# Kernel tuning notes

Hardware: AMD Instinct MI355X
Metric: run time of the kernel (lower is better)

## Reference

```python
import jax, jax.numpy as jnp
import numpy as np

VOCAB = 50000
D = 256        # embedding_dim = nb_head * size_per_head
H = 8          # nb_head
DH = 32        # size_per_head
B = 8192
L = 64


def setup_inputs() -> dict:
    key = jax.random.key(0)
    ks = jax.random.split(key, 8)
    tokens = jax.random.randint(ks[0], (B, L), 0, VOCAB)
    scale = 0.02
    emb_table = jax.random.normal(ks[1], (VOCAB, D), dtype=jnp.float32) * scale
    WQ = jax.random.normal(ks[2], (D, D), dtype=jnp.float32) * scale
    WK = jax.random.normal(ks[3], (D, D), dtype=jnp.float32) * scale
    WV = jax.random.normal(ks[4], (D, D), dtype=jnp.float32) * scale
    WO = jax.random.normal(ks[5], (D, D), dtype=jnp.float32) * scale
    dense_w = jax.random.normal(ks[6], (D, 1), dtype=jnp.float32) * scale
    dense_b = jnp.zeros((1,), dtype=jnp.float32)
    return {"tokens": tokens, "emb_table": emb_table, "WQ": WQ, "WK": WK,
            "WV": WV, "WO": WO, "dense_w": dense_w, "dense_b": dense_b}


def _fastformer(x, WQ, WK, WV, WO):
    # x: [B, L, D]
    b, l, _ = x.shape
    Q = (x @ WQ).reshape(b, l, H, DH)
    K = (x @ WK).reshape(b, l, H, DH)
    V = (x @ WV).reshape(b, l, H, DH)
    global_q = jnp.mean(Q, axis=1, keepdims=True)   # [B,1,H,DH]
    global_k = jnp.mean(K, axis=1, keepdims=True)
    w = jnp.sum(global_q * K + global_k * Q, axis=-1)  # [B,L,H]
    w = jax.nn.softmax(w, axis=1)                       # softmax over seq
    context = (w[..., None] * V).reshape(b, l, D)
    return context @ WO


def reference(tokens, emb_table, WQ, WK, WV, WO, dense_w, dense_b):
    # NewsEncoder forward (inference: dropout = identity; masks computed but
    # unused by Fastformer.call, matching the original code).
    title_emb = emb_table[tokens]                       # [B,L,D]
    hidden = _fastformer(title_emb, WQ, WK, WV, WO)     # [B,L,D]
    scores = (hidden @ dense_w + dense_b)[..., 0]       # [B,L]
    attn = jax.nn.softmax(scores, axis=1)               # over seq
    news_vector = jnp.sum(hidden * attn[..., None], axis=1)  # [B,D]
    return news_vector
```

## Files before the change

### kernel.cpp

```cpp
#include <hip/hip_runtime.h>
#include <cstdint>


using f32x4  = __attribute__((ext_vector_type(4))) float;
using bf16x8 = __attribute__((ext_vector_type(8))) short;

__device__ __forceinline__ unsigned int pack2bf(float a, float b) {
  unsigned int ua = __builtin_bit_cast(unsigned int, a);
  unsigned int ub = __builtin_bit_cast(unsigned int, b);
  ua = (ua + 0x7fffu + ((ua >> 16) & 1u)) >> 16;
  ub = (ub + 0x7fffu + ((ub >> 16) & 1u)) >> 16;
  return ua | (ub << 16);
}
__device__ __forceinline__ unsigned short bf1(float a) {
  unsigned int ua = __builtin_bit_cast(unsigned int, a);
  ua = (ua + 0x7fffu + ((ua >> 16) & 1u)) >> 16;
  return (unsigned short)ua;
}
__device__ __forceinline__ float ubf(unsigned int u) {
  return __builtin_bit_cast(float, u << 16);
}
__device__ __forceinline__ void gload_lds16(const void* g, void* l) {
  __builtin_amdgcn_global_load_lds(
      (const __attribute__((address_space(1))) void*)g,
      (__attribute__((address_space(3))) void*)l, 16, 0, 0);
}

__global__ __launch_bounds__(256) void prep_kernel(const float* __restrict__ WV,
                                                   const float* __restrict__ WO,
                                                   const float* __restrict__ dw,
                                                   unsigned short* __restrict__ mbf) {
  __shared__ float wod[256];
  const int t = threadIdx.x;
  float acc = 0.f;
  for (int e = 0; e < 256; e += 4) {
    const float4 w4 = *(const float4*)(WO + (size_t)t * 256 + e);
    const float4 d4 = *(const float4*)(dw + e);
    acc += w4.x * d4.x + w4.y * d4.y + w4.z * d4.z + w4.w * d4.w;
  }
  wod[t] = acc;
  __syncthreads();
  for (int h = 0; h < 8; ++h) {
    float a = 0.f;
    for (int j = 0; j < 32; j += 4) {
      const float4 w4 = *(const float4*)(WV + (size_t)t * 256 + h * 32 + j);
      a += w4.x * wod[h*32+j] + w4.y * wod[h*32+j+1] + w4.z * wod[h*32+j+2] + w4.w * wod[h*32+j+3];
    }
    const float o = __shfl_xor(a, 1);
    if (!(t & 1)) ((unsigned int*)mbf)[h * 128 + (t >> 1)] = pack2bf(a, o);
  }
}

__global__ __launch_bounds__(256) void prep_T(const float* __restrict__ WQ,
                                              const float* __restrict__ WK,
                                              unsigned short* __restrict__ tkn) {
  __shared__ float ek[8][32], eq[8][32];
  const int t = threadIdx.x;
  const int n0 = blockIdx.x * 8;
  const int h  = n0 >> 8;
  {
    const int ei = t >> 5, j = t & 31;
    const int e = (n0 & 255) + ei;
    ek[ei][j] = WK[(size_t)e * 256 + h * 32 + j];
    eq[ei][j] = WQ[(size_t)e * 256 + h * 32 + j];
  }
  __syncthreads();
  float wqd[32], wkd[32];
#pragma unroll
  for (int j = 0; j < 32; j += 4) {
    *(float4*)(wqd + j) = *(const float4*)(WQ + (size_t)t * 256 + h * 32 + j);
    *(float4*)(wkd + j) = *(const float4*)(WK + (size_t)t * 256 + h * 32 + j);
  }
#pragma unroll
  for (int ei = 0; ei < 8; ++ei) {
    float a = 0.f;
#pragma unroll
    for (int j = 0; j < 32; ++j) a += wqd[j] * ek[ei][j] + wkd[j] * eq[ei][j];
    const float o = __shfl_xor(a, 1);
    if (!(t & 1)) ((unsigned int*)tkn)[(size_t)(n0 + ei) * 128 + (t >> 1)] = pack2bf(a, o);
  }
}

__global__ __launch_bounds__(256) void prep_P(const float* __restrict__ WV,
                                              const float* __restrict__ WO,
                                              unsigned short* __restrict__ ptb) {
  __shared__ float wvs[32][32];
  __shared__ float wos[32][256];
  const int t = threadIdx.x;
  const int h = blockIdx.x, d0 = blockIdx.y * 32;
  {
    const int dd = t >> 3, jq = (t & 7) * 4;
    *(float4*)(&wvs[dd][jq]) = *(const float4*)(WV + (size_t)(d0 + dd) * 256 + h * 32 + jq);
    const int c4 = (t & 63) * 4;
#pragma unroll
    for (int jj = 0; jj < 8; ++jj) {
      const int j = (t >> 6) * 8 + jj;
      *(float4*)(&wos[j][c4]) = *(const float4*)(WO + (size_t)(h * 32 + j) * 256 + c4);
    }
  }
  __syncthreads();
  const int n = t;
#pragma unroll 4
  for (int dd = 0; dd < 32; ++dd) {
    float a = 0.f;
#pragma unroll
    for (int j = 0; j < 32; ++j) a += wvs[dd][j] * wos[j][n];
    ptb[(size_t)n * 2048 + h * 256 + d0 + dd] = bf1(a);
  }
}

__global__ __launch_bounds__(256) void ebf_kernel(const float4* __restrict__ emb4,
                                                  uint2* __restrict__ out2, int n) {
  for (int i = blockIdx.x * 256 + threadIdx.x; i < n; i += gridDim.x * 256) {
    const float4 v = emb4[i];
    uint2 pk;
    pk.x = pack2bf(v.x, v.y);
    pk.y = pack2bf(v.z, v.w);
    out2[i] = pk;
  }
}

__global__ __launch_bounds__(256) void xbar_kernel(const int* __restrict__ tokens,
                                                   const unsigned short* __restrict__ ebf,
                                                   unsigned short* __restrict__ xbf) {
  __shared__ int tok[64];
  __shared__ float part[4][64][4];
  const int b = blockIdx.x, t = threadIdx.x;
  if (t < 64) tok[t] = tokens[b * 64 + t];
  __syncthreads();
  const int cp = t & 63, rg = t >> 6;
  const uint2* e2 = (const uint2*)ebf;
  float s0 = 0.f, s1 = 0.f, s2 = 0.f, s3 = 0.f;
#pragma unroll
  for (int ri = 0; ri < 16; ++ri) {
    const uint2 u = e2[(size_t)tok[rg * 16 + ri] * 64 + cp];
    s0 += ubf(u.x & 0xffffu); s1 += ubf(u.x >> 16);
    s2 += ubf(u.y & 0xffffu); s3 += ubf(u.y >> 16);
  }
  *(float4*)part[rg][cp] = make_float4(s0, s1, s2, s3);
  __syncthreads();
  if (t < 64) {
    const float4 p0 = *(const float4*)part[0][t];
    const float4 p1 = *(const float4*)part[1][t];
    const float4 p2 = *(const float4*)part[2][t];
    const float4 p3 = *(const float4*)part[3][t];
    const float a0 = (p0.x + p1.x + p2.x + p3.x) * (1.f / 64.f);
    const float a1 = (p0.y + p1.y + p2.y + p3.y) * (1.f / 64.f);
    const float a2 = (p0.z + p1.z + p2.z + p3.z) * (1.f / 64.f);
    const float a3 = (p0.w + p1.w + p2.w + p3.w) * (1.f / 64.f);
    uint2 pk;
    pk.x = pack2bf(a0, a1);
    pk.y = pack2bf(a2, a3);
    *(uint2*)((unsigned int*)xbf + (size_t)b * 128 + 2 * t) = pk;
  }
}

__global__ __launch_bounds__(256) void cgemm(const unsigned short* __restrict__ xbf,
                                             const unsigned short* __restrict__ tkn,
                                             unsigned short* __restrict__ cbf) {
  __shared__ unsigned short As[64 * 264];
  const int t = threadIdx.x;
  const int m0 = blockIdx.x * 64, n0 = blockIdx.y * 64;
#pragma unroll
  for (int it = 0; it < 8; ++it) {
    const int idx = it * 256 + t;
    const int row = idx >> 5, c = idx & 31;
    const uint4 v = *(const uint4*)(xbf + (size_t)(m0 + row) * 256 + c * 8);
    *(uint4*)(As + row * 264 + c * 8) = v;
  }
  __syncthreads();
  const int wv = t >> 6, l = t & 63;
  const int g = l >> 4, r = l & 15;
#pragma unroll
  for (int nt = 0; nt < 4; ++nt) {
    const int n = n0 + nt * 16 + r;
    f32x4 acc = {0.f, 0.f, 0.f, 0.f};
#pragma unroll
    for (int kk = 0; kk < 8; ++kk) {
      const bf16x8 a  = *(const bf16x8*)(As + (16 * wv + r) * 264 + kk * 32 + g * 8);
      const bf16x8 bb = *(const bf16x8*)(tkn + (size_t)n * 256 + kk * 32 + g * 8);
      acc = __builtin_amdgcn_mfma_f32_16x16x32_bf16(a, bb, acc, 0, 0, 0);
    }
#pragma unroll
    for (int i = 0; i < 4; ++i)
      cbf[(size_t)(m0 + 16 * wv + g * 4 + i) * 2048 + n] = bf1(acc[i]);
  }
}

__global__ __launch_bounds__(256) void main_kernel(const int* __restrict__ tokens,
                                                   const unsigned short* __restrict__ ebf,
                                                   const unsigned short* __restrict__ mbf,
                                                   const float* __restrict__ dense_b,
                                                   unsigned short* __restrict__ cbf) {
  __shared__ unsigned short xl[64 * 256];
  __shared__ float wslds[64 * 17];
  __shared__ unsigned short cfT[16 * 80];
  const int t = threadIdx.x;
  const int b = blockIdx.x;
  const int wv = t >> 6, l = t & 63;
  const int g = l >> 4, r = l & 15;
  {
    unsigned int* cz = (unsigned int*)(cfT + 8 * 80);
    for (int z = t; z < 320; z += 256) cz[z] = 0u;
  }
  {
    const int ln = t & 63;
#pragma unroll
    for (int it = 0; it < 8; ++it) {
      const int R0 = it * 8 + wv * 2;
      const int R  = R0 + (ln >> 5);
      const int j  = ln & 31;
      const int tk = tokens[b * 64 + R];
      const unsigned short* src = ebf + (size_t)tk * 256 + ((j ^ (R & 7)) << 3);
      gload_lds16(src, (void*)(xl + R0 * 256));
    }
  }
  __syncthreads();
  {
    const unsigned short* arow = xl + (16 * wv + r) * 256;
    const int sw = r & 7;
    const unsigned short* brow = (r < 8) ? (cbf + (size_t)b * 2048 + r * 256)
                                         : (mbf + (size_t)(r - 8) * 256);
    f32x4 acc = {0.f, 0.f, 0.f, 0.f};
#pragma unroll
    for (int kk = 0; kk < 8; ++kk) {
      const bf16x8 a  = *(const bf16x8*)(arow + (((kk * 4 + g) ^ sw) << 3));
      const bf16x8 bb = *(const bf16x8*)(brow + kk * 32 + g * 8);
      acc = __builtin_amdgcn_mfma_f32_16x16x32_bf16(a, bb, acc, 0, 0, 0);
    }
#pragma unroll
    for (int i = 0; i < 4; ++i)
      wslds[(16 * wv + g * 4 + i) * 17 + r] = acc[i];
  }
  __syncthreads();
  {
#pragma unroll
    for (int hh = 0; hh < 2; ++hh) {
      const int h = 2 * wv + hh;
      const float v = wslds[l * 17 + h];
      float mx = v;
#pragma unroll
      for (int sft = 32; sft; sft >>= 1) mx = fmaxf(mx, __shfl_xor(mx, sft));
      const float e = expf(v - mx);
      float sm = e;
#pragma unroll
      for (int sft = 32; sft; sft >>= 1) sm += __shfl_xor(sm, sft);
      wslds[l * 17 + h] = e / sm;
    }
  }
  __syncthreads();
  {
    float p[8], sv[8];
#pragma unroll
    for (int h = 0; h < 8; ++h) { p[h] = wslds[l*17 + h]; sv[h] = wslds[l*17 + 8 + h]; }
    float sc = dense_b[0];
#pragma unroll
    for (int h = 0; h < 8; ++h) sc += p[h] * sv[h];
    float mx = sc;
#pragma unroll
    for (int sft = 32; sft; sft >>= 1) mx = fmaxf(mx, __shfl_xor(mx, sft));
    const float e = expf(sc - mx);
    float sm = e;
#pragma unroll
    for (int sft = 32; sft; sft >>= 1) sm += __shfl_xor(sm, sft);
    const float attn = e / sm;
    float cc0, cc1;
    if      (wv == 0) { cc0 = attn * p[0]; cc1 = attn * p[1]; }
    else if (wv == 1) { cc0 = attn * p[2]; cc1 = attn * p[3]; }
    else if (wv == 2) { cc0 = attn * p[4]; cc1 = attn * p[5]; }
    else              { cc0 = attn * p[6]; cc1 = attn * p[7]; }
    cfT[(2 * wv) * 80 + l]     = bf1(cc0);
    cfT[(2 * wv + 1) * 80 + l] = bf1(cc1);
  }
  __syncthreads();
  {
    const bf16x8 a0 = *(const bf16x8*)(cfT + r * 80 + g * 8);
    const bf16x8 a1 = *(const bf16x8*)(cfT + r * 80 + 32 + g * 8);
    const short* xs = (const short*)xl;
#pragma unroll
    for (int nt = 0; nt < 4; ++nt) {
      const int d = wv * 64 + nt * 16 + r;
      short bv0[8], bv1[8];
#pragma unroll
      for (int j = 0; j < 8; ++j) {
        const int off = ((((d >> 3) ^ j) << 3) | (d & 7));
        bv0[j] = xs[(g * 8 + j) * 256 + off];
        bv1[j] = xs[(32 + g * 8 + j) * 256 + off];
      }
      f32x4 acc = {0.f, 0.f, 0.f, 0.f};
      acc = __builtin_amdgcn_mfma_f32_16x16x32_bf16(a0, *(const bf16x8*)bv0, acc, 0, 0, 0);
      acc = __builtin_amdgcn_mfma_f32_16x16x32_bf16(a1, *(const bf16x8*)bv1, acc, 0, 0, 0);
      if (g < 2) {
#pragma unroll
        for (int i = 0; i < 4; ++i) {
          const int h = g * 4 + i;
          cbf[(size_t)b * 2048 + h * 256 + d] = bf1(acc[i]);
        }
      }
    }
  }
}

__global__ __launch_bounds__(256) void pgemm(const unsigned short* __restrict__ cbf,
                                             const unsigned short* __restrict__ ptb,
                                             float* __restrict__ out) {
  __shared__ unsigned short As[32 * 264];
  const int t = threadIdx.x;
  const int m0 = blockIdx.x * 32, n0 = blockIdx.y * 64;
  const int wv = t >> 6, l = t & 63;
  const int g = l >> 4, r = l & 15;
  const int msub = wv & 1, nhalf = wv >> 1;
  f32x4 acc[2] = {};
  for (int kc = 0; kc < 8; ++kc) {
    __syncthreads();
#pragma unroll
    for (int it = 0; it < 4; ++it) {
      const int idx = it * 256 + t;
      const int row = idx >> 5, c = idx & 31;
      const uint4 v = *(const uint4*)(cbf + (size_t)(m0 + row) * 2048 + kc * 256 + c * 8);
      *(uint4*)(As + row * 264 + c * 8) = v;
    }
    __syncthreads();
#pragma unroll
    for (int kk = 0; kk < 8; ++kk) {
      const bf16x8 a = *(const bf16x8*)(As + (16 * msub + r) * 264 + kk * 32 + g * 8);
#pragma unroll
      for (int nt = 0; nt < 2; ++nt) {
        const int n = n0 + (nhalf * 2 + nt) * 16 + r;
        const bf16x8 bb = *(const bf16x8*)(ptb + (size_t)n * 2048 + kc * 256 + kk * 32 + g * 8);
        acc[nt] = __builtin_amdgcn_mfma_f32_16x16x32_bf16(a, bb, acc[nt], 0, 0, 0);
      }
    }
  }
#pragma unroll
  for (int nt = 0; nt < 2; ++nt) {
    const int n = n0 + (nhalf * 2 + nt) * 16 + r;
#pragma unroll
    for (int i = 0; i < 4; ++i)
      out[(size_t)(m0 + 16 * msub + g * 4 + i) * 256 + n] = acc[nt][i];
  }
}

extern "C" void kernel_launch(void* const* d_in, const int* in_sizes, int n_in,
                              void* d_out, int out_size, void* d_ws, size_t ws_size,
                              hipStream_t stream) {
  const int*   tokens = (const int*)d_in[0];
  const float* emb    = (const float*)d_in[1];
  const float* WQ     = (const float*)d_in[2];
  const float* WK     = (const float*)d_in[3];
  const float* WV     = (const float*)d_in[4];
  const float* WO     = (const float*)d_in[5];
  const float* dw     = (const float*)d_in[6];
  const float* db     = (const float*)d_in[7];
  float* out = (float*)d_out;

  unsigned short* base = (unsigned short*)d_ws;
  unsigned short* mbf  = base;
  unsigned short* xbf  = base + 2048;
  unsigned short* tkn  = xbf + (size_t)8192 * 256;
  unsigned short* cbf  = tkn + (size_t)2048 * 256;
  unsigned short* ebf  = cbf + (size_t)8192 * 2048;
  unsigned short* ptb  = ebf + (size_t)50000 * 256;

  const size_t need_bytes = (size_t)(2048 + 8192*256 + 2048*256 + 8192*2048
                                     + 50000*256 + 256*2048) * 2;
  if (ws_size < need_bytes) return;

  prep_kernel<<<dim3(1), dim3(256), 0, stream>>>(WV, WO, dw, mbf);
  prep_T<<<dim3(256), dim3(256), 0, stream>>>(WQ, WK, tkn);
  prep_P<<<dim3(8, 8), dim3(256), 0, stream>>>(WV, WO, ptb);
  ebf_kernel<<<dim3(2048), dim3(256), 0, stream>>>((const float4*)emb, (uint2*)ebf,
                                                   50000 * 64);
  xbar_kernel<<<dim3(8192), dim3(256), 0, stream>>>(tokens, ebf, xbf);
  cgemm<<<dim3(128, 32), dim3(256), 0, stream>>>(xbf, tkn, cbf);
  main_kernel<<<dim3(8192), dim3(256), 0, stream>>>(tokens, ebf, mbf, db, cbf);
  pgemm<<<dim3(256, 4), dim3(256), 0, stream>>>(cbf, ptb, out);
}
```

Measured before the change: 275.1 us.

## Merge weight-prep kernels, widen xbar gathers, rotate store order in main kernel

The three small weight-preprocessing kernels are merged into one launch that dispatches on block index, removing two kernel launches and letting their blocks run concurrently. The xbar mean-gather kernel now loads 16-byte rows over 8 row groups instead of 8-byte rows over 4, and reduces through a larger shared buffer. In the main kernel the per-lane tile order is rotated by lane index so the scattered bf16 stores and LDS reads spread across addresses. The merged kernel reserves the largest shared-memory footprint for every block, and the wider gather uses more LDS.

```diff
diff --git a/kernel.cpp b/kernel.cpp
--- a/kernel.cpp
+++ b/kernel.cpp
@@ -26,86 +26,84 @@
       (__attribute__((address_space(3))) void*)l, 16, 0, 0);
 }
 
-__global__ __launch_bounds__(256) void prep_kernel(const float* __restrict__ WV,
-                                                   const float* __restrict__ WO,
-                                                   const float* __restrict__ dw,
-                                                   unsigned short* __restrict__ mbf) {
-  __shared__ float wod[256];
+__global__ __launch_bounds__(256) void prep_all(const float* __restrict__ WQ,
+                                                const float* __restrict__ WK,
+                                                const float* __restrict__ WV,
+                                                const float* __restrict__ WO,
+                                                const float* __restrict__ dw,
+                                                unsigned short* __restrict__ mbf,
+                                                unsigned short* __restrict__ tkn,
+                                                unsigned short* __restrict__ ptb) {
   const int t = threadIdx.x;
-  float acc = 0.f;
-  for (int e = 0; e < 256; e += 4) {
-    const float4 w4 = *(const float4*)(WO + (size_t)t * 256 + e);
-    const float4 d4 = *(const float4*)(dw + e);
-    acc += w4.x * d4.x + w4.y * d4.y + w4.z * d4.z + w4.w * d4.w;
-  }
-  wod[t] = acc;
-  __syncthreads();
-  for (int h = 0; h < 8; ++h) {
-    float a = 0.f;
+  const int bid = blockIdx.x;
+  if (bid == 0) {
+    __shared__ float wod[256];
+    float acc = 0.f;
+    for (int e = 0; e < 256; e += 4) {
+      const float4 w4 = *(const float4*)(WO + (size_t)t * 256 + e);
+      const float4 d4 = *(const float4*)(dw + e);
+      acc += w4.x * d4.x + w4.y * d4.y + w4.z * d4.z + w4.w * d4.w;
+    }
+    wod[t] = acc;
+    __syncthreads();
+    for (int h = 0; h < 8; ++h) {
+      float a = 0.f;
+      for (int j = 0; j < 32; j += 4) {
+        const float4 w4 = *(const float4*)(WV + (size_t)t * 256 + h * 32 + j);
+        a += w4.x * wod[h*32+j] + w4.y * wod[h*32+j+1] + w4.z * wod[h*32+j+2] + w4.w * wod[h*32+j+3];
+      }
+      const float o = __shfl_xor(a, 1);
+      if (!(t & 1)) ((unsigned int*)mbf)[h * 128 + (t >> 1)] = pack2bf(a, o);
+    }
+  } else if (bid <= 256) {
+    __shared__ float ek[8][32], eq[8][32];
+    const int n0 = (bid - 1) * 8;
+    const int h  = n0 >> 8;
+    {
+      const int ei = t >> 5, j = t & 31;
+      const int e = (n0 & 255) + ei;
+      ek[ei][j] = WK[(size_t)e * 256 + h * 32 + j];
+      eq[ei][j] = WQ[(size_t)e * 256 + h * 32 + j];
+    }
+    __syncthreads();
+    float wqd[32], wkd[32];
+#pragma unroll
     for (int j = 0; j < 32; j += 4) {
-      const float4 w4 = *(const float4*)(WV + (size_t)t * 256 + h * 32 + j);
-      a += w4.x * wod[h*32+j] + w4.y * wod[h*32+j+1] + w4.z * wod[h*32+j+2] + w4.w * wod[h*32+j+3];
-    }
-    const float o = __shfl_xor(a, 1);
-    if (!(t & 1)) ((unsigned int*)mbf)[h * 128 + (t >> 1)] = pack2bf(a, o);
-  }
-}
-
-__global__ __launch_bounds__(256) void prep_T(const float* __restrict__ WQ,
-                                              const float* __restrict__ WK,
-                                              unsigned short* __restrict__ tkn) {
-  __shared__ float ek[8][32], eq[8][32];
-  const int t = threadIdx.x;
-  const int n0 = blockIdx.x * 8;
-  const int h  = n0 >> 8;
-  {
-    const int ei = t >> 5, j = t & 31;
-    const int e = (n0 & 255) + ei;
-    ek[ei][j] = WK[(size_t)e * 256 + h * 32 + j];
-    eq[ei][j] = WQ[(size_t)e * 256 + h * 32 + j];
-  }
-  __syncthreads();
-  float wqd[32], wkd[32];
-#pragma unroll
-  for (int j = 0; j < 32; j += 4) {
-    *(float4*)(wqd + j) = *(const float4*)(WQ + (size_t)t * 256 + h * 32 + j);
-    *(float4*)(wkd + j) = *(const float4*)(WK + (size_t)t * 256 + h * 32 + j);
-  }
-#pragma unroll
-  for (int ei = 0; ei < 8; ++ei) {
-    float a = 0.f;
-#pragma unroll
-    for (int j = 0; j < 32; ++j) a += wqd[j] * ek[ei][j] + wkd[j] * eq[ei][j];
-    const float o = __shfl_xor(a, 1);
-    if (!(t & 1)) ((unsigned int*)tkn)[(size_t)(n0 + ei) * 128 + (t >> 1)] = pack2bf(a, o);
-  }
-}
-
-__global__ __launch_bounds__(256) void prep_P(const float* __restrict__ WV,
-                                              const float* __restrict__ WO,
-                                              unsigned short* __restrict__ ptb) {
-  __shared__ float wvs[32][32];
-  __shared__ float wos[32][256];
-  const int t = threadIdx.x;
-  const int h = blockIdx.x, d0 = blockIdx.y * 32;
-  {
-    const int dd = t >> 3, jq = (t & 7) * 4;
-    *(float4*)(&wvs[dd][jq]) = *(const float4*)(WV + (size_t)(d0 + dd) * 256 + h * 32 + jq);
-    const int c4 = (t & 63) * 4;
-#pragma unroll
-    for (int jj = 0; jj < 8; ++jj) {
-      const int j = (t >> 6) * 8 + jj;
-      *(float4*)(&wos[j][c4]) = *(const float4*)(WO + (size_t)(h * 32 + j) * 256 + c4);
-    }
-  }
-  __syncthreads();
-  const int n = t;
+      *(float4*)(wqd + j) = *(const float4*)(WQ + (size_t)t * 256 + h * 32 + j);
+      *(float4*)(wkd + j) = *(const float4*)(WK + (size_t)t * 256 + h * 32 + j);
+    }
+#pragma unroll
+    for (int ei = 0; ei < 8; ++ei) {
+      float a = 0.f;
+#pragma unroll
+      for (int j = 0; j < 32; ++j) a += wqd[j] * ek[ei][j] + wkd[j] * eq[ei][j];
+      const float o = __shfl_xor(a, 1);
+      if (!(t & 1)) ((unsigned int*)tkn)[(size_t)(n0 + ei) * 128 + (t >> 1)] = pack2bf(a, o);
+    }
+  } else {
+    __shared__ float wvs[32][32];
+    __shared__ float wos[32][256];
+    const int pb = bid - 257;
+    const int h = pb >> 3, d0 = (pb & 7) * 32;
+    {
+      const int dd = t >> 3, jq = (t & 7) * 4;
+      *(float4*)(&wvs[dd][jq]) = *(const float4*)(WV + (size_t)(d0 + dd) * 256 + h * 32 + jq);
+      const int c4 = (t & 63) * 4;
+#pragma unroll
+      for (int jj = 0; jj < 8; ++jj) {
+        const int j = (t >> 6) * 8 + jj;
+        *(float4*)(&wos[j][c4]) = *(const float4*)(WO + (size_t)(h * 32 + j) * 256 + c4);
+      }
+    }
+    __syncthreads();
+    const int n = t;
 #pragma unroll 4
-  for (int dd = 0; dd < 32; ++dd) {
-    float a = 0.f;
-#pragma unroll
-    for (int j = 0; j < 32; ++j) a += wvs[dd][j] * wos[j][n];
-    ptb[(size_t)n * 2048 + h * 256 + d0 + dd] = bf1(a);
+    for (int dd = 0; dd < 32; ++dd) {
+      float a = 0.f;
+#pragma unroll
+      for (int j = 0; j < 32; ++j) a += wvs[dd][j] * wos[j][n];
+      ptb[(size_t)n * 2048 + h * 256 + d0 + dd] = bf1(a);
+    }
   }
 }
 
@@ -124,35 +122,31 @@
                                                    const unsigned short* __restrict__ ebf,
                                                    unsigned short* __restrict__ xbf) {
   __shared__ int tok[64];
-  __shared__ float part[4][64][4];
+  __shared__ float part[8][256];
   const int b = blockIdx.x, t = threadIdx.x;
   if (t < 64) tok[t] = tokens[b * 64 + t];
   __syncthreads();
-  const int cp = t & 63, rg = t >> 6;
-  const uint2* e2 = (const uint2*)ebf;
-  float s0 = 0.f, s1 = 0.f, s2 = 0.f, s3 = 0.f;
-#pragma unroll
-  for (int ri = 0; ri < 16; ++ri) {
-    const uint2 u = e2[(size_t)tok[rg * 16 + ri] * 64 + cp];
-    s0 += ubf(u.x & 0xffffu); s1 += ubf(u.x >> 16);
-    s2 += ubf(u.y & 0xffffu); s3 += ubf(u.y >> 16);
-  }
-  *(float4*)part[rg][cp] = make_float4(s0, s1, s2, s3);
-  __syncthreads();
-  if (t < 64) {
-    const float4 p0 = *(const float4*)part[0][t];
-    const float4 p1 = *(const float4*)part[1][t];
-    const float4 p2 = *(const float4*)part[2][t];
-    const float4 p3 = *(const float4*)part[3][t];
-    const float a0 = (p0.x + p1.x + p2.x + p3.x) * (1.f / 64.f);
-    const float a1 = (p0.y + p1.y + p2.y + p3.y) * (1.f / 64.f);
-    const float a2 = (p0.z + p1.z + p2.z + p3.z) * (1.f / 64.f);
-    const float a3 = (p0.w + p1.w + p2.w + p3.w) * (1.f / 64.f);
-    uint2 pk;
-    pk.x = pack2bf(a0, a1);
-    pk.y = pack2bf(a2, a3);
-    *(uint2*)((unsigned int*)xbf + (size_t)b * 128 + 2 * t) = pk;
-  }
+  const int rg = t >> 5;
+  const int c16 = t & 31;
+  const uint4* e4 = (const uint4*)ebf;
+  float s[8] = {};
+#pragma unroll
+  for (int ri = 0; ri < 8; ++ri) {
+    const uint4 u = e4[(size_t)tok[rg * 8 + ri] * 32 + c16];
+    s[0] += ubf(u.x & 0xffffu); s[1] += ubf(u.x >> 16);
+    s[2] += ubf(u.y & 0xffffu); s[3] += ubf(u.y >> 16);
+    s[4] += ubf(u.z & 0xffffu); s[5] += ubf(u.z >> 16);
+    s[6] += ubf(u.w & 0xffffu); s[7] += ubf(u.w >> 16);
+  }
+#pragma unroll
+  for (int j = 0; j < 8; ++j) part[rg][c16 * 8 + j] = s[j];
+  __syncthreads();
+  float a = 0.f;
+#pragma unroll
+  for (int rg2 = 0; rg2 < 8; ++rg2) a += part[rg2][t];
+  a *= (1.f / 64.f);
+  const float o = __shfl_xor(a, 1);
+  if (!(t & 1)) ((unsigned int*)xbf)[(size_t)b * 128 + (t >> 1)] = pack2bf(a, o);
 }
 
 __global__ __launch_bounds__(256) void cgemm(const unsigned short* __restrict__ xbf,
@@ -278,7 +272,8 @@
     const bf16x8 a1 = *(const bf16x8*)(cfT + r * 80 + 32 + g * 8);
     const short* xs = (const short*)xl;
 #pragma unroll
-    for (int nt = 0; nt < 4; ++nt) {
+    for (int ntt = 0; ntt < 4; ++ntt) {
+      const int nt = (ntt + r) & 3;
       const int d = wv * 64 + nt * 16 + r;
       short bv0[8], bv1[8];
 #pragma unroll
@@ -366,9 +361,7 @@
                                      + 50000*256 + 256*2048) * 2;
   if (ws_size < need_bytes) return;
 
-  prep_kernel<<<dim3(1), dim3(256), 0, stream>>>(WV, WO, dw, mbf);
-  prep_T<<<dim3(256), dim3(256), 0, stream>>>(WQ, WK, tkn);
-  prep_P<<<dim3(8, 8), dim3(256), 0, stream>>>(WV, WO, ptb);
+  prep_all<<<dim3(321), dim3(256), 0, stream>>>(WQ, WK, WV, WO, dw, mbf, tkn, ptb);
   ebf_kernel<<<dim3(2048), dim3(256), 0, stream>>>((const float4*)emb, (uint2*)ebf,
                                                    50000 * 64);
   xbar_kernel<<<dim3(8192), dim3(256), 0, stream>>>(tokens, ebf, xbf);
```

Result: faster. 260.7 us (-5.2%).
